# Optimization experiments

Measured on AMD Instinct MI355X. Metric: run time of the kernel, lower is better.

Reference implementation:

```python
import jax, jax.numpy as jnp
import numpy as np

EPS = 1e-13

def masked_softmax(scores, mask):
    # scores: (B, L1, L2), mask: (B, L2) float {0,1}
    m = mask[:, None, :]
    # faithful to ESIM masked_softmax: softmax(scores * mask), re-mask, renormalize
    p = jax.nn.softmax(scores * m, axis=-1) * m
    return p / (jnp.sum(p, axis=-1, keepdims=True) + EPS)

def weighted_sum(values, weights, mask):
    # values: (B, Lv, H), weights: (B, Lq, Lv), mask: (B, Lq)
    out = jnp.einsum('bqv,bvh->bqh', weights, values)
    return out * mask[:, :, None]

def setup_inputs() -> dict:
    key = jax.random.key(0)
    k1, k2, k3, k4 = jax.random.split(key, 4)
    B, P, Q, H = 64, 1024, 1024, 256
    pre_batch = jax.random.normal(k1, (B, P, H), dtype=jnp.float32)
    hypo_batch = jax.random.normal(k2, (B, Q, H), dtype=jnp.float32)
    pre_mask = jax.random.randint(k3, (B, P), 0, 2, dtype=jnp.int32).at[:, 0].set(1)
    hypo_mask = jax.random.randint(k4, (B, Q), 0, 2, dtype=jnp.int32).at[:, 0].set(1)
    return {"pre_batch": pre_batch, "pre_mask": pre_mask,
            "hypo_batch": hypo_batch, "hypo_mask": hypo_mask}

def reference(pre_batch, pre_mask, hypo_batch, hypo_mask):
    pre_m = pre_mask.astype(pre_batch.dtype)
    hypo_m = hypo_mask.astype(hypo_batch.dtype)
    # similarity: (B, P, Q)
    similarity = jnp.einsum('bph,bqh->bpq', pre_batch, hypo_batch)
    pre_hypo_attn = masked_softmax(similarity, hypo_m)                       # (B,P,Q)
    hypo_pre_attn = masked_softmax(jnp.swapaxes(similarity, 1, 2), pre_m)    # (B,Q,P)
    attented_pre = weighted_sum(hypo_batch, pre_hypo_attn, pre_m)            # (B,P,H)
    attented_hypo = weighted_sum(pre_batch, hypo_pre_attn, hypo_m)           # (B,Q,H)
    return (attented_pre, attented_hypo)
```

## Files before the change

### kernel.cpp

```cpp
#include <hip/hip_runtime.h>
#include <stdint.h>

#define NB 64
#define NN 1024
#define NH 256

typedef _Float16 h8v __attribute__((ext_vector_type(8)));
typedef float    f4v __attribute__((ext_vector_type(4)));
typedef uint32_t u4v __attribute__((ext_vector_type(4)));
typedef uint32_t u2v __attribute__((ext_vector_type(2)));

static __device__ __forceinline__ uint32_t pack2h(float a, float b) {
  uint32_t ua = (uint32_t)__builtin_bit_cast(uint16_t, (_Float16)a);
  uint32_t ub = (uint32_t)__builtin_bit_cast(uint16_t, (_Float16)b);
  return ua | (ub << 16);
}

static __device__ __forceinline__ void gl_lds16(const void* g, void* l) {
  __builtin_amdgcn_global_load_lds(
      (const __attribute__((address_space(1))) uint32_t*)g,
      (__attribute__((address_space(3))) uint32_t*)l, 16, 0, 0);
}

__global__ __launch_bounds__(256)
void prep_tiles(const float* __restrict__ pre, const float* __restrict__ hypo,
                uint8_t* __restrict__ img)
{
  const int id = blockIdx.x;
  const int m  = id >> 11;
  const int bt = id & 2047;
  const float* src = (m ? hypo : pre) + (size_t)bt * (32 * NH);
  uint8_t* kimg = img + (size_t)id * 32768;
  uint8_t* vimg = kimg + 16384;

  __shared__ __align__(16) float ft[32 * 260];
  const int t = threadIdx.x, w = t >> 6, lane = t & 63;

#pragma unroll
  for (int i = 0; i < 8; ++i) {
    const int row = w * 8 + i;
    gl_lds16(src + row * NH + lane * 4, (uint8_t*)ft + row * 1040);
  }
  __syncthreads();

#pragma unroll
  for (int c = 0; c < 4; ++c) {
    const int k = c * 8 + (t >> 5);
    const uint32_t X = (uint32_t)((t & 31) * 16);
    const uint32_t h0 = ((X >> 4) ^ (uint32_t)(k & 7)) * 8;
    const uint8_t* p = (const uint8_t*)ft + k * 1040 + h0 * 4;
    f4v a0 = *(const f4v*)p;
    f4v a1 = *(const f4v*)(p + 16);
    u4v o; o[0] = pack2h(a0[0], a0[1]); o[1] = pack2h(a0[2], a0[3]);
    o[2] = pack2h(a1[0], a1[1]); o[3] = pack2h(a1[2], a1[3]);
    *(u4v*)(kimg + c * 4096 + t * 16) = o;
  }
#pragma unroll
  for (int c = 0; c < 4; ++c) {
    const int h  = c * 64 + (t >> 2);
    const int k8 = 8 * (t & 3);
    float v[8];
#pragma unroll
    for (int j = 0; j < 8; ++j) v[j] = ft[(k8 + j) * 260 + h];
    u4v o; o[0] = pack2h(v[0], v[1]); o[1] = pack2h(v[2], v[3]);
    o[2] = pack2h(v[4], v[5]); o[3] = pack2h(v[6], v[7]);
    *(u4v*)(vimg + c * 4096 + t * 16) = o;
  }
}

__global__ __launch_bounds__(256, 2)
void attn_img(const uint8_t* __restrict__ img,
              const int* __restrict__ pre_mask, const int* __restrict__ hypo_mask,
              float* __restrict__ out)
{
  const int fid  = blockIdx.x;
  const int xcd  = fid & 7;
  const int s    = fid >> 3;
  const int bp   = xcd * 16 + (s >> 3);
  const int rblk = s & 7;
  const int pass = bp >> 6;
  const int b    = bp & 63;

  const uint8_t* qimg  = img + (size_t)(pass ? 1 : 0) * 67108864;
  const uint8_t* kvimg = img + (size_t)(pass ? 0 : 1) * 67108864;
  const int* kmask = pass == 0 ? hypo_mask : pre_mask;
  const int* qmask = pass == 0 ? pre_mask  : hypo_mask;
  float* outp = out + ((size_t)pass * NB + b) * NN * NH;
  const uint8_t* kvb = kvimg + (size_t)b * (32 * 32768);
  const int* kmb = kmask + b * NN;

  __shared__ __align__(16) uint8_t sbuf[2][32768];

  const int t    = threadIdx.x;
  const int lane = t & 63;
  const int w    = t >> 6;
  const int g    = lane >> 4;
  const int q    = lane & 15;

  h8v qf0[8], qf1[8];
  {
    const uint8_t* qb = qimg + (size_t)b * (32 * 32768);
#pragma unroll
    for (int ff = 0; ff < 2; ++ff) {
      const int qrow = rblk * 128 + w * 32 + ff * 16 + q;
      const uint8_t* qt = qb + (size_t)(qrow >> 5) * 32768 + (qrow & 31) * 512;
      const uint32_t swq = (uint32_t)((qrow & 7) << 4);
#pragma unroll
      for (int c = 0; c < 8; ++c) {
        h8v v = *(const h8v*)(qt + (((uint32_t)((c * 4 + g) << 4)) ^ swq));
        if (ff == 0) qf0[c] = v; else qf1[c] = v;
      }
    }
  }

  f4v accA[16], accB[16];
#pragma unroll
  for (int cf = 0; cf < 16; ++cf) { accA[cf] = (f4v){0,0,0,0}; accB[cf] = (f4v){0,0,0,0}; }
  float mrunA = -1e30f, lrunA = 0.f, mrunB = -1e30f, lrunB = 0.f;

#pragma unroll
  for (int i = 0; i < 8; ++i)
    gl_lds16(kvb + w * 8192 + i * 1024 + lane * 16, &sbuf[0][0] + w * 8192 + i * 1024);
  __syncthreads();

#pragma unroll 1
  for (int kt = 0; kt < 32; ++kt) {
    const int cur = kt & 1;
    if (kt < 31) {
      const uint8_t* kvt = kvb + (size_t)(kt + 1) * 32768;
#pragma unroll
      for (int i = 0; i < 8; ++i)
        gl_lds16(kvt + w * 8192 + i * 1024 + lane * 16,
                 &sbuf[cur ^ 1][0] + w * 8192 + i * 1024);
    }
    const uint8_t* sK = &sbuf[cur][0];
    const uint8_t* sV = sK + 16384;
    const int kb = kt * 32;

    int msk0[4], msk1[4];
#pragma unroll
    for (int r = 0; r < 4; ++r) {
      msk0[r] = kmb[kb + 4 * g + r];
      msk1[r] = kmb[kb + 16 + 4 * g + r];
    }

    f4v s0A = (f4v){0,0,0,0}, s1A = (f4v){0,0,0,0};
    f4v s0B = (f4v){0,0,0,0}, s1B = (f4v){0,0,0,0};
    __builtin_amdgcn_s_setprio(1);
#pragma unroll
    for (int c = 0; c < 8; ++c) {
      const uint32_t a0 = (uint32_t)(q * 512) + (((uint32_t)(c * 64 + g * 16)) ^ ((uint32_t)((q & 7) << 4)));
      h8v k0 = *(const h8v*)(sK + a0);
      h8v k1 = *(const h8v*)(sK + a0 + 8192);
      s0A = __builtin_amdgcn_mfma_f32_16x16x32_f16(k0, qf0[c], s0A, 0, 0, 0);
      s0B = __builtin_amdgcn_mfma_f32_16x16x32_f16(k0, qf1[c], s0B, 0, 0, 0);
      s1A = __builtin_amdgcn_mfma_f32_16x16x32_f16(k1, qf0[c], s1A, 0, 0, 0);
      s1B = __builtin_amdgcn_mfma_f32_16x16x32_f16(k1, qf1[c], s1B, 0, 0, 0);
    }
    __builtin_amdgcn_s_setprio(0);

    float tA = -1e30f, tB = -1e30f;
#pragma unroll
    for (int r = 0; r < 4; ++r) {
      tA = fmaxf(tA, fmaxf(msk0[r] ? s0A[r] : -1e30f, msk1[r] ? s1A[r] : -1e30f));
      tB = fmaxf(tB, fmaxf(msk0[r] ? s0B[r] : -1e30f, msk1[r] ? s1B[r] : -1e30f));
    }
    tA = fmaxf(tA, __shfl_xor(tA, 16));  tB = fmaxf(tB, __shfl_xor(tB, 16));
    tA = fmaxf(tA, __shfl_xor(tA, 32));  tB = fmaxf(tB, __shfl_xor(tB, 32));

    const bool grow = __any(fmaxf(tA - mrunA, tB - mrunB) > 8.0f);
    if (grow) {
      const float mnA = fmaxf(mrunA, tA), mnB = fmaxf(mrunB, tB);
      const float sA = __expf(mrunA - mnA), sB = __expf(mrunB - mnB);
      mrunA = mnA; mrunB = mnB;
      lrunA *= sA; lrunB *= sB;
      float srA[4], srB[4];
#pragma unroll
      for (int r = 0; r < 4; ++r) {
        srA[r] = __shfl(sA, 4 * g + r);
        srB[r] = __shfl(sB, 4 * g + r);
      }
#pragma unroll
      for (int cf = 0; cf < 16; ++cf) {
#pragma unroll
        for (int r = 0; r < 4; ++r) {
          accA[cf][r] *= srA[r];
          accB[cf][r] *= srB[r];
        }
      }
    }

    float pA[8], pB[8];
    float psA = 0.f, psB = 0.f;
#pragma unroll
    for (int r = 0; r < 4; ++r) {
      float a0 = msk0[r] ? __expf(s0A[r] - mrunA) : 0.f;
      float a1 = msk1[r] ? __expf(s1A[r] - mrunA) : 0.f;
      float b0 = msk0[r] ? __expf(s0B[r] - mrunB) : 0.f;
      float b1 = msk1[r] ? __expf(s1B[r] - mrunB) : 0.f;
      pA[r] = a0; pA[4 + r] = a1; psA += a0 + a1;
      pB[r] = b0; pB[4 + r] = b1; psB += b0 + b1;
    }
    psA += __shfl_xor(psA, 16);  psB += __shfl_xor(psB, 16);
    psA += __shfl_xor(psA, 32);  psB += __shfl_xor(psB, 32);
    lrunA += psA; lrunB += psB;

    h8v apA, apB;
    {
      const int srcA = q + 16 * ((2 * g) & 3);
      const int srcB = srcA + 16;
      uint32_t Af00 = pack2h(pA[0], pA[1]), Af01 = pack2h(pA[2], pA[3]);
      uint32_t Af10 = pack2h(pA[4], pA[5]), Af11 = pack2h(pA[6], pA[7]);
      uint32_t Bf00 = pack2h(pB[0], pB[1]), Bf01 = pack2h(pB[2], pB[3]);
      uint32_t Bf10 = pack2h(pB[4], pB[5]), Bf11 = pack2h(pB[6], pB[7]);
      uint32_t Aw0a = __shfl(Af00, srcA), Aw1a = __shfl(Af01, srcA);
      uint32_t Aw0b = __shfl(Af00, srcB), Aw1b = __shfl(Af01, srcB);
      uint32_t Ax0a = __shfl(Af10, srcA), Ax1a = __shfl(Af11, srcA);
      uint32_t Ax0b = __shfl(Af10, srcB), Ax1b = __shfl(Af11, srcB);
      uint32_t Bw0a = __shfl(Bf00, srcA), Bw1a = __shfl(Bf01, srcA);
      uint32_t Bw0b = __shfl(Bf00, srcB), Bw1b = __shfl(Bf01, srcB);
      uint32_t Bx0a = __shfl(Bf10, srcA), Bx1a = __shfl(Bf11, srcA);
      uint32_t Bx0b = __shfl(Bf10, srcB), Bx1b = __shfl(Bf11, srcB);
      u4v au, bu;
      au[0] = (g >= 2) ? Ax0a : Aw0a;
      au[1] = (g >= 2) ? Ax1a : Aw1a;
      au[2] = (g >= 2) ? Ax0b : Aw0b;
      au[3] = (g >= 2) ? Ax1b : Aw1b;
      bu[0] = (g >= 2) ? Bx0a : Bw0a;
      bu[1] = (g >= 2) ? Bx1a : Bw1a;
      bu[2] = (g >= 2) ? Bx0b : Bw0b;
      bu[3] = (g >= 2) ? Bx1b : Bw1b;
      apA = __builtin_bit_cast(h8v, au);
      apB = __builtin_bit_cast(h8v, bu);
    }

    __builtin_amdgcn_s_setprio(1);
#pragma unroll
    for (int cf = 0; cf < 16; ++cf) {
      h8v bv = *(const h8v*)(sV + (uint32_t)((cf * 16 + q) * 64 + g * 16));
      accA[cf] = __builtin_amdgcn_mfma_f32_16x16x32_f16(apA, bv, accA[cf], 0, 0, 0);
      accB[cf] = __builtin_amdgcn_mfma_f32_16x16x32_f16(apB, bv, accB[cf], 0, 0, 0);
    }
    __builtin_amdgcn_s_setprio(0);

    __syncthreads();
  }

#pragma unroll
  for (int ff = 0; ff < 2; ++ff) {
    const float lrun = ff ? lrunB : lrunA;
    float fac[4];
#pragma unroll
    for (int r = 0; r < 4; ++r) {
      const float lr = __shfl(lrun, 4 * g + r);
      const int row = rblk * 128 + w * 32 + ff * 16 + 4 * g + r;
      fac[r] = (float)qmask[b * NN + row] / lr;
    }
    float* op = outp + (size_t)(rblk * 128 + w * 32 + ff * 16) * NH;
#pragma unroll
    for (int cf = 0; cf < 16; ++cf) {
#pragma unroll
      for (int r = 0; r < 4; ++r) {
        float v = ff ? accB[cf][r] : accA[cf][r];
        op[(4 * g + r) * NH + cf * 16 + q] = v * fac[r];
      }
    }
  }
}

__global__ __launch_bounds__(256, 2)
void fused_dual_attn_fb(const float* __restrict__ pre,  const int* __restrict__ pre_mask,
                        const float* __restrict__ hypo, const int* __restrict__ hypo_mask,
                        float* __restrict__ out)
{
  const int pass = blockIdx.z;
  const float* Qm  = pass == 0 ? pre  : hypo;
  const float* KVm = pass == 0 ? hypo : pre;
  const int* kmask = pass == 0 ? hypo_mask : pre_mask;
  const int* qmask = pass == 0 ? pre_mask  : hypo_mask;
  float* outp = out + (size_t)pass * NB * NN * NH;

  const int b  = blockIdx.y;
  const int r0 = blockIdx.x * 64;

  __shared__ __align__(16) unsigned char sK [32 * NH * 2];
  __shared__ __align__(16) unsigned char sVt[NH * 16 * 4];
  __shared__ int smask[NN];

  const int t    = threadIdx.x;
  const int lane = t & 63;
  const int w    = t >> 6;
  const int g    = lane >> 4;
  const int q    = lane & 15;

  for (int i = t; i < NN; i += 256) smask[i] = kmask[b * NN + i];

  const int qrow = r0 + w * 16 + q;
  h8v qf[8];
  {
    const float* qp = Qm + ((size_t)b * NN + qrow) * NH + g * 8;
#pragma unroll
    for (int c = 0; c < 8; ++c) {
      f4v a0 = *(const f4v*)(qp + c * 32);
      f4v a1 = *(const f4v*)(qp + c * 32 + 4);
      h8v v;
      v[0] = (_Float16)a0[0]; v[1] = (_Float16)a0[1];
      v[2] = (_Float16)a0[2]; v[3] = (_Float16)a0[3];
      v[4] = (_Float16)a1[0]; v[5] = (_Float16)a1[1];
      v[6] = (_Float16)a1[2]; v[7] = (_Float16)a1[3];
      qf[c] = v;
    }
  }

  f4v acc[16];
#pragma unroll
  for (int cf = 0; cf < 16; ++cf) acc[cf] = (f4v){0.f, 0.f, 0.f, 0.f};
  float mrun = -1e30f, lrun = 0.f;

  const int skey = t & 31;
  const int m16  = (t >> 1) & 15;
  const int scb  = (t >> 5) << 2;
  const int odd  = skey & 1;

  for (int kb = 0; kb < NN; kb += 32) {
    __syncthreads();
#pragma unroll
    for (int i = 0; i < 8; ++i) {
      const int col = scb + 32 * i;
      f4v v = *(const f4v*)(KVm + ((size_t)b * NN + kb + skey) * NH + col);
      u2v d; d[0] = pack2h(v[0], v[1]); d[1] = pack2h(v[2], v[3]);
      uint32_t ka = (uint32_t)(skey * 512 + col * 2) ^ (uint32_t)((skey & 7) << 4);
      *(u2v*)(sK + ka) = d;
      float e = odd ? v[0] : v[2];
      float f = odd ? v[1] : v[3];
      float oe = __shfl_xor(e, 1);
      float of = __shfl_xor(f, 1);
      float lo0 = odd ? oe   : v[0];
      float hi0 = odd ? v[2] : oe;
      float lo1 = odd ? of   : v[1];
      float hi1 = odd ? v[3] : of;
      const int h0 = col + odd * 2;
      *(uint32_t*)(sVt + (uint32_t)((h0    ) * 64 + m16 * 4)) = pack2h(lo0, hi0);
      *(uint32_t*)(sVt + (uint32_t)((h0 + 1) * 64 + m16 * 4)) = pack2h(lo1, hi1);
    }
    __syncthreads();

    f4v s0 = (f4v){0.f,0.f,0.f,0.f}, s1 = (f4v){0.f,0.f,0.f,0.f};
#pragma unroll
    for (int c = 0; c < 8; ++c) {
      uint32_t a0 = ((uint32_t)(q * 512 + c * 64 + g * 16)) ^ (uint32_t)((q & 7) << 4);
      uint32_t a1 = ((uint32_t)((16 + q) * 512 + c * 64 + g * 16)) ^ (uint32_t)((q & 7) << 4);
      h8v k0 = *(const h8v*)(sK + a0);
      h8v k1 = *(const h8v*)(sK + a1);
      s0 = __builtin_amdgcn_mfma_f32_16x16x32_f16(k0, qf[c], s0, 0, 0, 0);
      s1 = __builtin_amdgcn_mfma_f32_16x16x32_f16(k1, qf[c], s1, 0, 0, 0);
    }

    int msk[8];
#pragma unroll
    for (int r = 0; r < 4; ++r) {
      msk[r]     = smask[kb + 4 * g + r];
      msk[4 + r] = smask[kb + 16 + 4 * g + r];
    }
    float tmax = -1e30f;
#pragma unroll
    for (int r = 0; r < 4; ++r)
      tmax = fmaxf(tmax, fmaxf(msk[r] ? s0[r] : -1e30f, msk[4 + r] ? s1[r] : -1e30f));
    tmax = fmaxf(tmax, __shfl_xor(tmax, 16));
    tmax = fmaxf(tmax, __shfl_xor(tmax, 32));
    const float mnew = fmaxf(mrun, tmax);
    const float scl = __expf(mrun - mnew);
    mrun = mnew;

    float p[8];
    float psum = 0.f;
#pragma unroll
    for (int r = 0; r < 4; ++r) {
      float p0 = msk[r]     ? __expf(s0[r] - mnew) : 0.f;
      float p1 = msk[4 + r] ? __expf(s1[r] - mnew) : 0.f;
      p[r] = p0; p[4 + r] = p1;
      psum += p0 + p1;
    }
    psum += __shfl_xor(psum, 16);
    psum += __shfl_xor(psum, 32);
    lrun = lrun * scl + psum;

    float srow[4];
#pragma unroll
    for (int r = 0; r < 4; ++r) srow[r] = __shfl(scl, 4 * g + r);
#pragma unroll
    for (int cf = 0; cf < 16; ++cf) {
#pragma unroll
      for (int r = 0; r < 4; ++r) acc[cf][r] *= srow[r];
    }

    uint32_t pf00 = pack2h(p[0], p[1]);
    uint32_t pf01 = pack2h(p[2], p[3]);
    uint32_t pf10 = pack2h(p[4], p[5]);
    uint32_t pf11 = pack2h(p[6], p[7]);
    const int srcA = q + 16 * ((2 * g) & 3);
    const int srcB = srcA + 16;
    uint32_t w0a = __shfl(pf00, srcA), w1a = __shfl(pf01, srcA);
    uint32_t w0b = __shfl(pf00, srcB), w1b = __shfl(pf01, srcB);
    uint32_t x0a = __shfl(pf10, srcA), x1a = __shfl(pf11, srcA);
    uint32_t x0b = __shfl(pf10, srcB), x1b = __shfl(pf11, srcB);
    u4v au;
    au[0] = (g >= 2) ? x0a : w0a;
    au[1] = (g >= 2) ? x1a : w1a;
    au[2] = (g >= 2) ? x0b : w0b;
    au[3] = (g >= 2) ? x1b : w1b;
    const h8v ap = __builtin_bit_cast(h8v, au);

#pragma unroll
    for (int cf = 0; cf < 16; ++cf) {
      h8v bv = *(const h8v*)(sVt + (uint32_t)((cf * 16 + q) * 64 + g * 16));
      acc[cf] = __builtin_amdgcn_mfma_f32_16x16x32_f16(ap, bv, acc[cf], 0, 0, 0);
    }
  }

  float fac[4];
#pragma unroll
  for (int r = 0; r < 4; ++r) {
    const float lr = __shfl(lrun, 4 * g + r);
    const int row = r0 + w * 16 + 4 * g + r;
    fac[r] = (float)qmask[b * NN + row] / lr;
  }
  float* op = outp + ((size_t)b * NN + r0 + w * 16) * NH;
#pragma unroll
  for (int cf = 0; cf < 16; ++cf) {
#pragma unroll
    for (int r = 0; r < 4; ++r) {
      op[(4 * g + r) * NH + cf * 16 + q] = acc[cf][r] * fac[r];
    }
  }
}

extern "C" void kernel_launch(void* const* d_in, const int* in_sizes, int n_in,
                              void* d_out, int out_size, void* d_ws, size_t ws_size,
                              hipStream_t stream) {
  const float* pre       = (const float*)d_in[0];
  const int*   pre_mask  = (const int*)d_in[1];
  const float* hypo      = (const float*)d_in[2];
  const int*   hypo_mask = (const int*)d_in[3];
  float* out = (float*)d_out;
  (void)in_sizes; (void)n_in; (void)out_size;

  if (ws_size >= (size_t)2 * 67108864) {
    uint8_t* img = (uint8_t*)d_ws;
    prep_tiles<<<dim3(4096), dim3(256), 0, stream>>>(pre, hypo, img);
    attn_img<<<dim3(1024), dim3(256), 0, stream>>>(img, pre_mask, hypo_mask, out);
  } else {
    fused_dual_attn_fb<<<dim3(16, 64, 2), dim3(256), 0, stream>>>(pre, pre_mask, hypo, hypo_mask, out);
  }
}
```

Before: 236.4 us.

## Fold log2e into fp16 images, use exp2, bias-init masks, relayout V

The prep kernel now scales the fp16 images by the square root of log2(e), so each Q·K dot product comes out already in base 2 and the softmax can use exp2 instead of expf. The key mask becomes an additive bias table in LDS that seeds the MFMA accumulators, which removes the per-element mask selects and the global mask loads inside the loop. The V image is stored in a new layout so the per-tile B-operand LDS reads are contiguous across lanes, which should reduce bank conflicts. This costs an extra 4 KB of LDS per block and slightly changes fp16 rounding of the scaled inputs.

```diff
diff --git a/kernel.cpp b/kernel.cpp
--- a/kernel.cpp
+++ b/kernel.cpp
@@ -4,6 +4,7 @@
 #define NB 64
 #define NN 1024
 #define NH 256
+#define KSCALE 1.20112240878645f
 
 typedef _Float16 h8v __attribute__((ext_vector_type(8)));
 typedef float    f4v __attribute__((ext_vector_type(4)));
@@ -51,20 +52,25 @@
     const uint8_t* p = (const uint8_t*)ft + k * 1040 + h0 * 4;
     f4v a0 = *(const f4v*)p;
     f4v a1 = *(const f4v*)(p + 16);
-    u4v o; o[0] = pack2h(a0[0], a0[1]); o[1] = pack2h(a0[2], a0[3]);
-    o[2] = pack2h(a1[0], a1[1]); o[3] = pack2h(a1[2], a1[3]);
+    u4v o;
+    o[0] = pack2h(a0[0] * KSCALE, a0[1] * KSCALE);
+    o[1] = pack2h(a0[2] * KSCALE, a0[3] * KSCALE);
+    o[2] = pack2h(a1[0] * KSCALE, a1[1] * KSCALE);
+    o[3] = pack2h(a1[2] * KSCALE, a1[3] * KSCALE);
     *(u4v*)(kimg + c * 4096 + t * 16) = o;
   }
-#pragma unroll
-  for (int c = 0; c < 4; ++c) {
-    const int h  = c * 64 + (t >> 2);
-    const int k8 = 8 * (t & 3);
-    float v[8];
-#pragma unroll
-    for (int j = 0; j < 8; ++j) v[j] = ft[(k8 + j) * 260 + h];
-    u4v o; o[0] = pack2h(v[0], v[1]); o[1] = pack2h(v[2], v[3]);
-    o[2] = pack2h(v[4], v[5]); o[3] = pack2h(v[6], v[7]);
-    *(u4v*)(vimg + c * 4096 + t * 16) = o;
+  {
+    const int u = t >> 6;
+#pragma unroll
+    for (int c = 0; c < 4; ++c) {
+      const int h = c * 64 + (t & 63);
+      float v[8];
+#pragma unroll
+      for (int j = 0; j < 8; ++j) v[j] = ft[(8 * u + j) * 260 + h];
+      u4v o; o[0] = pack2h(v[0], v[1]); o[1] = pack2h(v[2], v[3]);
+      o[2] = pack2h(v[4], v[5]); o[3] = pack2h(v[6], v[7]);
+      *(u4v*)(vimg + u * 4096 + h * 16) = o;
+    }
   }
 }
 
@@ -90,6 +96,7 @@
   const int* kmb = kmask + b * NN;
 
   __shared__ __align__(16) uint8_t sbuf[2][32768];
+  __shared__ __align__(16) float sbias[NN];
 
   const int t    = threadIdx.x;
   const int lane = t & 63;
@@ -97,6 +104,8 @@
   const int g    = lane >> 4;
   const int q    = lane & 15;
 
+  for (int i = t; i < NN; i += 256) sbias[i] = kmb[i] ? 0.f : -1e30f;
+
   h8v qf0[8], qf1[8];
   {
     const uint8_t* qb = qimg + (size_t)b * (32 * 32768);
@@ -137,15 +146,10 @@
     const uint8_t* sV = sK + 16384;
     const int kb = kt * 32;
 
-    int msk0[4], msk1[4];
-#pragma unroll
-    for (int r = 0; r < 4; ++r) {
-      msk0[r] = kmb[kb + 4 * g + r];
-      msk1[r] = kmb[kb + 16 + 4 * g + r];
-    }
-
-    f4v s0A = (f4v){0,0,0,0}, s1A = (f4v){0,0,0,0};
-    f4v s0B = (f4v){0,0,0,0}, s1B = (f4v){0,0,0,0};
+    const f4v cin0 = *(const f4v*)&sbias[kb + 4 * g];
+    const f4v cin1 = *(const f4v*)&sbias[kb + 16 + 4 * g];
+
+    f4v s0A = cin0, s1A = cin1, s0B = cin0, s1B = cin1;
     __builtin_amdgcn_s_setprio(1);
 #pragma unroll
     for (int c = 0; c < 8; ++c) {
@@ -162,8 +166,8 @@
     float tA = -1e30f, tB = -1e30f;
 #pragma unroll
     for (int r = 0; r < 4; ++r) {
-      tA = fmaxf(tA, fmaxf(msk0[r] ? s0A[r] : -1e30f, msk1[r] ? s1A[r] : -1e30f));
-      tB = fmaxf(tB, fmaxf(msk0[r] ? s0B[r] : -1e30f, msk1[r] ? s1B[r] : -1e30f));
+      tA = fmaxf(tA, fmaxf(s0A[r], s1A[r]));
+      tB = fmaxf(tB, fmaxf(s0B[r], s1B[r]));
     }
     tA = fmaxf(tA, __shfl_xor(tA, 16));  tB = fmaxf(tB, __shfl_xor(tB, 16));
     tA = fmaxf(tA, __shfl_xor(tA, 32));  tB = fmaxf(tB, __shfl_xor(tB, 32));
@@ -171,7 +175,7 @@
     const bool grow = __any(fmaxf(tA - mrunA, tB - mrunB) > 8.0f);
     if (grow) {
       const float mnA = fmaxf(mrunA, tA), mnB = fmaxf(mrunB, tB);
-      const float sA = __expf(mrunA - mnA), sB = __expf(mrunB - mnB);
+      const float sA = __builtin_exp2f(mrunA - mnA), sB = __builtin_exp2f(mrunB - mnB);
       mrunA = mnA; mrunB = mnB;
       lrunA *= sA; lrunB *= sB;
       float srA[4], srB[4];
@@ -194,10 +198,10 @@
     float psA = 0.f, psB = 0.f;
 #pragma unroll
     for (int r = 0; r < 4; ++r) {
-      float a0 = msk0[r] ? __expf(s0A[r] - mrunA) : 0.f;
-      float a1 = msk1[r] ? __expf(s1A[r] - mrunA) : 0.f;
-      float b0 = msk0[r] ? __expf(s0B[r] - mrunB) : 0.f;
-      float b1 = msk1[r] ? __expf(s1B[r] - mrunB) : 0.f;
+      float a0 = __builtin_exp2f(s0A[r] - mrunA);
+      float a1 = __builtin_exp2f(s1A[r] - mrunA);
+      float b0 = __builtin_exp2f(s0B[r] - mrunB);
+      float b1 = __builtin_exp2f(s1B[r] - mrunB);
       pA[r] = a0; pA[4 + r] = a1; psA += a0 + a1;
       pB[r] = b0; pB[4 + r] = b1; psB += b0 + b1;
     }
@@ -237,7 +241,7 @@
     __builtin_amdgcn_s_setprio(1);
 #pragma unroll
     for (int cf = 0; cf < 16; ++cf) {
-      h8v bv = *(const h8v*)(sV + (uint32_t)((cf * 16 + q) * 64 + g * 16));
+      h8v bv = *(const h8v*)(sV + (uint32_t)(g * 4096 + (cf * 16 + q) * 16));
       accA[cf] = __builtin_amdgcn_mfma_f32_16x16x32_f16(apA, bv, accA[cf], 0, 0, 0);
       accB[cf] = __builtin_amdgcn_mfma_f32_16x16x32_f16(apB, bv, accB[cf], 0, 0, 0);
     }
```

Result: slower. 254.8 us (+7.8%).

## Transpose PV MFMA so probabilities feed B operand directly, removing shuffles

Applied to the files above, without the earlier changes.

Swaps the operand roles in the P·V MFMA so V becomes the A operand and the softmax probabilities, already held per lane in the score layout, become the B operand without cross-lane shuffles. The V image preprocessing is rearranged to match the new operand layout, and rescaling and normalization now use per-lane scalars instead of shuffled per-row values. As a side effect, output stores become 16-byte vector writes per row. This removes many ds_bpermute shuffles per iteration, but any mismatch between the new V image layout and the MFMA operand mapping would give wrong results.

```diff
diff --git a/kernel.cpp b/kernel.cpp
--- a/kernel.cpp
+++ b/kernel.cpp
@@ -55,16 +55,20 @@
     o[2] = pack2h(a1[0], a1[1]); o[3] = pack2h(a1[2], a1[3]);
     *(u4v*)(kimg + c * 4096 + t * 16) = o;
   }
-#pragma unroll
-  for (int c = 0; c < 4; ++c) {
-    const int h  = c * 64 + (t >> 2);
-    const int k8 = 8 * (t & 3);
-    float v[8];
-#pragma unroll
-    for (int j = 0; j < 8; ++j) v[j] = ft[(k8 + j) * 260 + h];
-    u4v o; o[0] = pack2h(v[0], v[1]); o[1] = pack2h(v[2], v[3]);
-    o[2] = pack2h(v[4], v[5]); o[3] = pack2h(v[6], v[7]);
-    *(u4v*)(vimg + c * 4096 + t * 16) = o;
+  {
+    const int g2 = t >> 6;
+#pragma unroll
+    for (int c = 0; c < 4; ++c) {
+      const int h = c * 64 + (t & 63);
+      float v[8];
+#pragma unroll
+      for (int j = 0; j < 4; ++j) v[j]     = ft[(4 * g2 + j) * 260 + h];
+#pragma unroll
+      for (int j = 0; j < 4; ++j) v[4 + j] = ft[(16 + 4 * g2 + j) * 260 + h];
+      u4v o; o[0] = pack2h(v[0], v[1]); o[1] = pack2h(v[2], v[3]);
+      o[2] = pack2h(v[4], v[5]); o[3] = pack2h(v[6], v[7]);
+      *(u4v*)(vimg + g2 * 4096 + h * 16) = o;
+    }
   }
 }
 
@@ -174,18 +178,12 @@
       const float sA = __expf(mrunA - mnA), sB = __expf(mrunB - mnB);
       mrunA = mnA; mrunB = mnB;
       lrunA *= sA; lrunB *= sB;
-      float srA[4], srB[4];
-#pragma unroll
-      for (int r = 0; r < 4; ++r) {
-        srA[r] = __shfl(sA, 4 * g + r);
-        srB[r] = __shfl(sB, 4 * g + r);
-      }
 #pragma unroll
       for (int cf = 0; cf < 16; ++cf) {
 #pragma unroll
         for (int r = 0; r < 4; ++r) {
-          accA[cf][r] *= srA[r];
-          accB[cf][r] *= srB[r];
+          accA[cf][r] *= sA;
+          accB[cf][r] *= sB;
         }
       }
     }
@@ -205,41 +203,20 @@
     psA += __shfl_xor(psA, 32);  psB += __shfl_xor(psB, 32);
     lrunA += psA; lrunB += psB;
 
-    h8v apA, apB;
-    {
-      const int srcA = q + 16 * ((2 * g) & 3);
-      const int srcB = srcA + 16;
-      uint32_t Af00 = pack2h(pA[0], pA[1]), Af01 = pack2h(pA[2], pA[3]);
-      uint32_t Af10 = pack2h(pA[4], pA[5]), Af11 = pack2h(pA[6], pA[7]);
-      uint32_t Bf00 = pack2h(pB[0], pB[1]), Bf01 = pack2h(pB[2], pB[3]);
-      uint32_t Bf10 = pack2h(pB[4], pB[5]), Bf11 = pack2h(pB[6], pB[7]);
-      uint32_t Aw0a = __shfl(Af00, srcA), Aw1a = __shfl(Af01, srcA);
-      uint32_t Aw0b = __shfl(Af00, srcB), Aw1b = __shfl(Af01, srcB);
-      uint32_t Ax0a = __shfl(Af10, srcA), Ax1a = __shfl(Af11, srcA);
-      uint32_t Ax0b = __shfl(Af10, srcB), Ax1b = __shfl(Af11, srcB);
-      uint32_t Bw0a = __shfl(Bf00, srcA), Bw1a = __shfl(Bf01, srcA);
-      uint32_t Bw0b = __shfl(Bf00, srcB), Bw1b = __shfl(Bf01, srcB);
-      uint32_t Bx0a = __shfl(Bf10, srcA), Bx1a = __shfl(Bf11, srcA);
-      uint32_t Bx0b = __shfl(Bf10, srcB), Bx1b = __shfl(Bf11, srcB);
-      u4v au, bu;
-      au[0] = (g >= 2) ? Ax0a : Aw0a;
-      au[1] = (g >= 2) ? Ax1a : Aw1a;
-      au[2] = (g >= 2) ? Ax0b : Aw0b;
-      au[3] = (g >= 2) ? Ax1b : Aw1b;
-      bu[0] = (g >= 2) ? Bx0a : Bw0a;
-      bu[1] = (g >= 2) ? Bx1a : Bw1a;
-      bu[2] = (g >= 2) ? Bx0b : Bw0b;
-      bu[3] = (g >= 2) ? Bx1b : Bw1b;
-      apA = __builtin_bit_cast(h8v, au);
-      apB = __builtin_bit_cast(h8v, bu);
-    }
+    u4v au, bu;
+    au[0] = pack2h(pA[0], pA[1]); au[1] = pack2h(pA[2], pA[3]);
+    au[2] = pack2h(pA[4], pA[5]); au[3] = pack2h(pA[6], pA[7]);
+    bu[0] = pack2h(pB[0], pB[1]); bu[1] = pack2h(pB[2], pB[3]);
+    bu[2] = pack2h(pB[4], pB[5]); bu[3] = pack2h(pB[6], pB[7]);
+    const h8v apA = __builtin_bit_cast(h8v, au);
+    const h8v apB = __builtin_bit_cast(h8v, bu);
 
     __builtin_amdgcn_s_setprio(1);
 #pragma unroll
     for (int cf = 0; cf < 16; ++cf) {
-      h8v bv = *(const h8v*)(sV + (uint32_t)((cf * 16 + q) * 64 + g * 16));
-      accA[cf] = __builtin_amdgcn_mfma_f32_16x16x32_f16(apA, bv, accA[cf], 0, 0, 0);
-      accB[cf] = __builtin_amdgcn_mfma_f32_16x16x32_f16(apB, bv, accB[cf], 0, 0, 0);
+      h8v av = *(const h8v*)(sV + (uint32_t)(g * 4096 + (cf * 16 + q) * 16));
+      accA[cf] = __builtin_amdgcn_mfma_f32_16x16x32_f16(av, apA, accA[cf], 0, 0, 0);
+      accB[cf] = __builtin_amdgcn_mfma_f32_16x16x32_f16(av, apB, accB[cf], 0, 0, 0);
     }
     __builtin_amdgcn_s_setprio(0);
 
@@ -249,21 +226,14 @@
 #pragma unroll
   for (int ff = 0; ff < 2; ++ff) {
     const float lrun = ff ? lrunB : lrunA;
-    float fac[4];
-#pragma unroll
-    for (int r = 0; r < 4; ++r) {
-      const float lr = __shfl(lrun, 4 * g + r);
-      const int row = rblk * 128 + w * 32 + ff * 16 + 4 * g + r;
-      fac[r] = (float)qmask[b * NN + row] / lr;
-    }
-    float* op = outp + (size_t)(rblk * 128 + w * 32 + ff * 16) * NH;
+    const int qrow = rblk * 128 + w * 32 + ff * 16 + q;
+    const float fac = (float)qmask[b * NN + qrow] / lrun;
+    float* op = outp + (size_t)qrow * NH;
 #pragma unroll
     for (int cf = 0; cf < 16; ++cf) {
-#pragma unroll
-      for (int r = 0; r < 4; ++r) {
-        float v = ff ? accB[cf][r] : accA[cf][r];
-        op[(4 * g + r) * NH + cf * 16 + q] = v * fac[r];
-      }
+      f4v v = ff ? accB[cf] : accA[cf];
+      v[0] *= fac; v[1] *= fac; v[2] *= fac; v[3] *= fac;
+      *(f4v*)(op + cf * 16 + 4 * g) = v;
     }
   }
 }
```

Result: faster. 224.3 us (-5.1%).
